# Kernel optimization log

Measured on AMD Instinct MI355X. Metric: run time of the kernel, lower is better.

## Reference

```python
import jax, jax.numpy as jnp
import numpy as np

B, T, C = 512, 2048, 32

def setup_inputs() -> dict:
    key = jax.random.key(0)
    k1, k2, k3, k4 = jax.random.split(key, 4)
    target_predict = jax.random.normal(k1, (B, T, C), dtype=jnp.float32)
    trans = jax.random.uniform(k2, (C, C), dtype=jnp.float32)
    # labels in [0, C]; label value C is the padded class dropped by [:, :, :-1]
    target_true = jax.random.randint(k3, (B, T), 0, C + 1, dtype=jnp.int64)
    lens = jax.random.randint(k4, (B,), 0, T, dtype=jnp.int64)
    return {"target_predict": target_predict, "trans": trans,
            "target_true": target_true, "lens": lens}

def reference(target_predict, trans, target_true, lens):
    dt = target_predict.dtype
    c = trans.shape[0]
    # one_hot with depth C+1, drop last column (pad class) -> [B, T, C]
    oh = jax.nn.one_hot(target_true, c + 1, dtype=dt)[:, :, :-1]
    # emission score of the true path
    sum_h = jnp.sum(target_predict * oh, axis=(1, 2))  # [B]
    # g_mtx[b,t,i,j] = sum_k trans[i,k]*pre[b,t,k]*fut[b,t,j]; summed over t,i,j
    pre, fut = oh[:, :-1, :], oh[:, 1:, :]
    sum_g = jnp.einsum('ik,btk,btj->b', trans, pre, fut)  # [B]
    # forward-algorithm partition via scan; carry Z_col [B, C]
    lens_f = lens.astype(dt)
    Z_col0 = target_predict[:, 0, :]
    emis = jnp.swapaxes(target_predict[:, 1:, :], 0, 1)  # [T-1, B, C]
    steps = jnp.arange(1, target_predict.shape[1], dtype=dt)
    def step(Z_col, xs):
        e_t, t = xs
        valid = (lens_f >= t).astype(dt)  # [B]
        # Z_t[b,p,q] = Z_col[b,p] + (e_t[b,q] + trans[p,q]) * mask[b]
        Zt = Z_col[:, :, None] + (e_t[:, None, :] + trans) * valid[:, None, None]
        Z_sum = jax.scipy.special.logsumexp(Zt, axis=2)  # [B, C]
        Z_col_new = jnp.where(valid[:, None] > 0, Z_sum, Z_col)
        return Z_col_new, None
    Z_col, _ = jax.lax.scan(step, Z_col0, (emis, steps))
    # final Z_t is Z_col broadcast along last axis -> sum over [1,2] = C * sum(Z_col)
    sum_Z = jnp.asarray(c, dt) * jnp.sum(Z_col, axis=1)  # [B]
    return jnp.mean(sum_Z - sum_h - sum_g)
```

## Files before the change

kernel.cpp:

```cpp
#include <hip/hip_runtime.h>
#include <stdint.h>

#define BDIM 512
#define TDIM 2048
#define CDIM 32
#define BLOCK 256
#define CHUNKS (TDIM / BLOCK)
#define NBLK (BDIM * CHUNKS)

using bf16x8 = __attribute__((ext_vector_type(8))) short;
using f32x16 = __attribute__((ext_vector_type(16))) float;
using f32x4  = __attribute__((ext_vector_type(4))) float;

__device__ inline unsigned short f2bf(float f) {
    uint32_t u = __builtin_bit_cast(uint32_t, f);
    u += 0x7fff + ((u >> 16) & 1);
    return (unsigned short)(u >> 16);
}


__global__ __launch_bounds__(BLOCK) void crf_main(
        const float* __restrict__ P, const int* __restrict__ TT,
        const int* __restrict__ LEN, const float* __restrict__ trans,
        float* __restrict__ partials) {
    __shared__ unsigned short sEb[CDIM * CDIM];
    __shared__ float sCol[CDIM];
    __shared__ unsigned short epBuf[4 * 4 * 64 * 8];

    const int tid  = threadIdx.x;
    const int lane = tid & 63;
    const int wid  = tid >> 6;

    #pragma unroll
    for (int q = 0; q < 4; ++q) {
        int i = q * BLOCK + tid;
        sEb[i] = f2bf(__expf(trans[i]));
    }
    if (tid < CDIM) {
        float s = 0.f;
        #pragma unroll
        for (int r = 0; r < CDIM; ++r) s += trans[r * CDIM + tid];
        sCol[tid] = s;
    }
    __syncthreads();

    bf16x8 bB0, bB1;
    {
        const int n  = lane & 31;
        const int kh = (lane >> 5) * 8;
        bB0 = *reinterpret_cast<const bf16x8*>(&sEb[n * CDIM + 0  + kh]);
        bB1 = *reinterpret_cast<const bf16x8*>(&sEb[n * CDIM + 16 + kh]);
    }

    const int blk   = blockIdx.x;
    const int b     = blk >> 3;
    const int chunk = blk & 7;
    const int t     = chunk * BLOCK + tid;
    const int len   = LEN[b];
    const long rowbase = ((long)b * TDIM + t) * CDIM;

    const int tt  = TT[b * TDIM + t];
    const int tt2 = (t < TDIM - 1) ? TT[b * TDIM + t + 1] : CDIM;

    float h = 0.f, g = 0.f;
    if (tt < CDIM) {
        h = P[rowbase + tt];
        if (tt2 < CDIM) g = sCol[tt];
    }

    float zpart = 0.f;
    const int tbase = chunk * BLOCK + wid * 64;

    if (tbase <= len) {
        const bool heavy = (t >= 1) && (t <= len);
        float p[CDIM];
        if (heavy || t == 0) {
            const f32x4* row4 = reinterpret_cast<const f32x4*>(P + rowbase);
            #pragma unroll
            for (int q = 0; q < 8; ++q) {
                f32x4 v = row4[q];
                p[4*q+0] = v[0]; p[4*q+1] = v[1]; p[4*q+2] = v[2]; p[4*q+3] = v[3];
            }
        } else {
            #pragma unroll
            for (int y = 0; y < CDIM; ++y) p[y] = 0.f;
        }
        if (t == 0) {
            float s = 0.f;
            #pragma unroll
            for (int y = 0; y < CDIM; ++y) s += p[y];
            zpart += 32.f * s;
        }

        unsigned short* epW = epBuf + wid * (4 * 64 * 8);
        #pragma unroll
        for (int c = 0; c < 4; ++c) {
            union { bf16x8 v; unsigned short u[8]; } pk;
            #pragma unroll
            for (int j = 0; j < 8; ++j) {
                float e = heavy ? __expf(p[c * 8 + j]) : 0.f;
                pk.u[j] = f2bf(e);
            }
            *reinterpret_cast<bf16x8*>(&epW[(c * 64 + lane) * 8]) = pk.v;
        }

        float zlog = 0.f;
        const int chi = lane >> 5;
        #pragma unroll
        for (int T = 0; T < 2; ++T) {
            const int m = T * 32 + (lane & 31);
            bf16x8 a0 = *reinterpret_cast<const bf16x8*>(&epW[((0 + chi) * 64 + m) * 8]);
            bf16x8 a1 = *reinterpret_cast<const bf16x8*>(&epW[((2 + chi) * 64 + m) * 8]);
            f32x16 acc = {};
            acc = __builtin_amdgcn_mfma_f32_32x32x16_bf16(a0, bB0, acc, 0, 0, 0);
            acc = __builtin_amdgcn_mfma_f32_32x32x16_bf16(a1, bB1, acc, 0, 0, 0);
            #pragma unroll
            for (int r = 0; r < 16; ++r) {
                const int row  = (r & 3) + 8 * (r >> 2) + 4 * chi + T * 32;
                const int trow = tbase + row;
                const bool valid = (trow >= 1) && (trow <= len);
                zlog += valid ? __log2f(acc[r]) : 0.f;
            }
        }
        zpart += 32.f * 0.6931471805599453f * zlog;
    }

    float v = zpart - h - g;
    #pragma unroll
    for (int off = 32; off; off >>= 1) v += __shfl_down(v, off);
    __shared__ float red[BLOCK / 64];
    if (lane == 0) red[wid] = v;
    __syncthreads();
    if (tid == 0)
        partials[blk] = red[0] + red[1] + red[2] + red[3];
}

__global__ void crf_finish(const float* __restrict__ partials, float* __restrict__ out) {
    double s = 0.0;
    for (int i = threadIdx.x; i < NBLK; i += 256) s += (double)partials[i];
    #pragma unroll
    for (int off = 32; off; off >>= 1) s += __shfl_down(s, off);
    __shared__ double red[4];
    if ((threadIdx.x & 63) == 0) red[threadIdx.x >> 6] = s;
    __syncthreads();
    if (threadIdx.x == 0) out[0] = (float)((red[0] + red[1] + red[2] + red[3]) / (double)BDIM);
}

extern "C" void kernel_launch(void* const* d_in, const int* in_sizes, int n_in,
                              void* d_out, int out_size, void* d_ws, size_t ws_size,
                              hipStream_t stream) {
    const float* P     = (const float*)d_in[0];
    const float* trans = (const float*)d_in[1];
    const int*   TT    = (const int*)d_in[2];
    const int*   LEN   = (const int*)d_in[3];
    float* out = (float*)d_out;
    float* ws  = (float*)d_ws;
    float* partials = ws + 2048;

    hipLaunchKernelGGL(crf_main,   dim3(NBLK), dim3(BLOCK), 0, stream, P, TT, LEN, trans, partials);
    hipLaunchKernelGGL(crf_finish, dim3(1),    dim3(256),   0, stream, partials, out);
}
```

Baseline: 204.4 us.

## Skip trans setup in padded blocks, swizzle LDS, pair logs, widen finish reduce

Blocks whose whole time chunk lies past the sequence length now skip the exp(trans) bf16 table build and the B-fragment load. The LDS staging buffer for exponentiated emissions gets an XOR swizzle to cut bank conflicts on the MFMA A-operand reads. Log2 calls are halved by multiplying adjacent accumulator values before taking the log, which risks overflow or underflow in float. The final reduction kernel uses 1024 threads instead of 256.

```diff
diff --git a/kernel.cpp b/kernel.cpp
--- a/kernel.cpp
+++ b/kernel.cpp
@@ -5,7 +5,7 @@
 #define TDIM 2048
 #define CDIM 32
 #define BLOCK 256
-#define CHUNKS (TDIM / BLOCK)
+#define CHUNKS 8
 #define NBLK (BDIM * CHUNKS)
 
 using bf16x8 = __attribute__((ext_vector_type(8))) short;
@@ -18,6 +18,10 @@
     return (unsigned short)(u >> 16);
 }
 
+__device__ inline int swz16(int row) {
+    return (row << 4) ^ (((row >> 3) & 3) << 4);
+}
+
 
 __global__ __launch_bounds__(BLOCK) void crf_main(
         const float* __restrict__ P, const int* __restrict__ TT,
@@ -25,32 +29,11 @@
         float* __restrict__ partials) {
     __shared__ unsigned short sEb[CDIM * CDIM];
     __shared__ float sCol[CDIM];
-    __shared__ unsigned short epBuf[4 * 4 * 64 * 8];
+    __shared__ char epBuf[4 * 4 * 1024];
 
     const int tid  = threadIdx.x;
     const int lane = tid & 63;
     const int wid  = tid >> 6;
-
-    #pragma unroll
-    for (int q = 0; q < 4; ++q) {
-        int i = q * BLOCK + tid;
-        sEb[i] = f2bf(__expf(trans[i]));
-    }
-    if (tid < CDIM) {
-        float s = 0.f;
-        #pragma unroll
-        for (int r = 0; r < CDIM; ++r) s += trans[r * CDIM + tid];
-        sCol[tid] = s;
-    }
-    __syncthreads();
-
-    bf16x8 bB0, bB1;
-    {
-        const int n  = lane & 31;
-        const int kh = (lane >> 5) * 8;
-        bB0 = *reinterpret_cast<const bf16x8*>(&sEb[n * CDIM + 0  + kh]);
-        bB1 = *reinterpret_cast<const bf16x8*>(&sEb[n * CDIM + 16 + kh]);
-    }
 
     const int blk   = blockIdx.x;
     const int b     = blk >> 3;
@@ -58,6 +41,31 @@
     const int t     = chunk * BLOCK + tid;
     const int len   = LEN[b];
     const long rowbase = ((long)b * TDIM + t) * CDIM;
+
+    const bool blockHeavy = (chunk * BLOCK) <= len;
+
+    if (tid < CDIM) {
+        float s = 0.f;
+        #pragma unroll
+        for (int r = 0; r < CDIM; ++r) s += trans[r * CDIM + tid];
+        sCol[tid] = s;
+    }
+    if (blockHeavy) {
+        #pragma unroll
+        for (int q = 0; q < 4; ++q) {
+            int i = q * BLOCK + tid;
+            sEb[i] = f2bf(__expf(trans[i]));
+        }
+    }
+    __syncthreads();
+
+    bf16x8 bB0, bB1;
+    if (blockHeavy) {
+        const int n  = lane & 31;
+        const int kh = (lane >> 5) * 8;
+        bB0 = *reinterpret_cast<const bf16x8*>(&sEb[n * CDIM + 0  + kh]);
+        bB1 = *reinterpret_cast<const bf16x8*>(&sEb[n * CDIM + 16 + kh]);
+    }
 
     const int tt  = TT[b * TDIM + t];
     const int tt2 = (t < TDIM - 1) ? TT[b * TDIM + t + 1] : CDIM;
@@ -92,7 +100,7 @@
             zpart += 32.f * s;
         }
 
-        unsigned short* epW = epBuf + wid * (4 * 64 * 8);
+        char* epW = epBuf + wid * 4096;
         #pragma unroll
         for (int c = 0; c < 4; ++c) {
             union { bf16x8 v; unsigned short u[8]; } pk;
@@ -101,7 +109,7 @@
                 float e = heavy ? __expf(p[c * 8 + j]) : 0.f;
                 pk.u[j] = f2bf(e);
             }
-            *reinterpret_cast<bf16x8*>(&epW[(c * 64 + lane) * 8]) = pk.v;
+            *reinterpret_cast<bf16x8*>(epW + c * 1024 + swz16(lane)) = pk.v;
         }
 
         float zlog = 0.f;
@@ -109,18 +117,22 @@
         #pragma unroll
         for (int T = 0; T < 2; ++T) {
             const int m = T * 32 + (lane & 31);
-            bf16x8 a0 = *reinterpret_cast<const bf16x8*>(&epW[((0 + chi) * 64 + m) * 8]);
-            bf16x8 a1 = *reinterpret_cast<const bf16x8*>(&epW[((2 + chi) * 64 + m) * 8]);
+            bf16x8 a0 = *reinterpret_cast<const bf16x8*>(epW + (0 + chi) * 1024 + swz16(m));
+            bf16x8 a1 = *reinterpret_cast<const bf16x8*>(epW + (2 + chi) * 1024 + swz16(m));
             f32x16 acc = {};
             acc = __builtin_amdgcn_mfma_f32_32x32x16_bf16(a0, bB0, acc, 0, 0, 0);
             acc = __builtin_amdgcn_mfma_f32_32x32x16_bf16(a1, bB1, acc, 0, 0, 0);
+            float av[16];
             #pragma unroll
             for (int r = 0; r < 16; ++r) {
                 const int row  = (r & 3) + 8 * (r >> 2) + 4 * chi + T * 32;
                 const int trow = tbase + row;
                 const bool valid = (trow >= 1) && (trow <= len);
-                zlog += valid ? __log2f(acc[r]) : 0.f;
+                av[r] = valid ? acc[r] : 1.0f;
             }
+            #pragma unroll
+            for (int r = 0; r < 16; r += 2)
+                zlog += __log2f(av[r] * av[r + 1]);
         }
         zpart += 32.f * 0.6931471805599453f * zlog;
     }
@@ -135,15 +147,22 @@
         partials[blk] = red[0] + red[1] + red[2] + red[3];
 }
 
-__global__ void crf_finish(const float* __restrict__ partials, float* __restrict__ out) {
+__global__ __launch_bounds__(1024) void crf_finish(
+        const float* __restrict__ partials, float* __restrict__ out) {
+    const int tid = threadIdx.x;
     double s = 0.0;
-    for (int i = threadIdx.x; i < NBLK; i += 256) s += (double)partials[i];
+    for (int i = tid; i < NBLK; i += 1024) s += (double)partials[i];
     #pragma unroll
     for (int off = 32; off; off >>= 1) s += __shfl_down(s, off);
-    __shared__ double red[4];
-    if ((threadIdx.x & 63) == 0) red[threadIdx.x >> 6] = s;
+    __shared__ double red[16];
+    if ((tid & 63) == 0) red[tid >> 6] = s;
     __syncthreads();
-    if (threadIdx.x == 0) out[0] = (float)((red[0] + red[1] + red[2] + red[3]) / (double)BDIM);
+    if (tid == 0) {
+        double r = 0.0;
+        #pragma unroll
+        for (int w = 0; w < 16; ++w) r += red[w];
+        out[0] = (float)(r / (double)BDIM);
+    }
 }
 
 extern "C" void kernel_launch(void* const* d_in, const int* in_sizes, int n_in,
@@ -158,5 +177,5 @@
     float* partials = ws + 2048;
 
     hipLaunchKernelGGL(crf_main,   dim3(NBLK), dim3(BLOCK), 0, stream, P, TT, LEN, trans, partials);
-    hipLaunchKernelGGL(crf_finish, dim3(1),    dim3(256),   0, stream, partials, out);
+    hipLaunchKernelGGL(crf_finish, dim3(1),    dim3(1024),  0, stream, partials, out);
 }
```

Result: no change. 203.4 us (-0.5%).
